# Kernel tuning notes

Measured on AMD Instinct MI355X. Metric: run time of the kernel, lower is better.

The kernel has to match this reference:

```python
import jax, jax.numpy as jnp
import numpy as np

GRID_SIZE = 5
SPLINE_ORDER = 3
GRID_RANGE = (-1.0, 1.0)
BN_EPS = 1e-5


def _make_grid():
    h = (GRID_RANGE[1] - GRID_RANGE[0]) / GRID_SIZE
    # grid_size + 2*spline_order + 1 = 12 knots, shared across the 9 patch features
    return jnp.arange(-SPLINE_ORDER, GRID_SIZE + SPLINE_ORDER + 1, dtype=jnp.float32) * h + GRID_RANGE[0]


def _b_splines(x, grid):
    # x: (N, F) -> (N, F, grid_size + spline_order) via Cox-de Boor recursion
    x = x[..., None]
    bases = ((x >= grid[:-1]) & (x < grid[1:])).astype(x.dtype)
    for k in range(1, SPLINE_ORDER + 1):
        left = (x - grid[: -(k + 1)]) / (grid[k:-1] - grid[: -(k + 1)]) * bases[..., :-1]
        right = (grid[k + 1:] - x) / (grid[k + 1:] - grid[1:-k]) * bases[..., 1:]
        bases = left + right
    return bases


def setup_inputs() -> dict:
    key = jax.random.key(0)
    ks = jax.random.split(key, 4)
    B, C, H, W = 4, 64, 96, 96
    return {
        "x": jax.random.normal(ks[0], (B, C, H, W), dtype=jnp.float32),
        "base_weight": jax.random.normal(ks[1], (1, 9), dtype=jnp.float32) * 0.3,
        "spline_weight": jax.random.normal(ks[2], (1, 9, GRID_SIZE + SPLINE_ORDER), dtype=jnp.float32) * 0.3,
        "spline_scaler": jax.random.normal(ks[3], (1, 9), dtype=jnp.float32) * 0.3 + 1.0,
        "bn_gamma": jnp.ones((C,), dtype=jnp.float32),
        "bn_beta": jnp.zeros((C,), dtype=jnp.float32),
    }


def reference(x, base_weight, spline_weight, spline_scaler, bn_gamma, bn_beta):
    B, C, H, W = x.shape
    grid = _make_grid()
    # Per-channel depthwise 3x3 patch extraction (pad 1, stride 1), shared KANLinear(9 -> 1)
    patches = jax.lax.conv_general_dilated_patches(
        x.reshape(B * C, 1, H, W), (3, 3), (1, 1), [(1, 1), (1, 1)]
    )  # (B*C, 9, H, W)
    tok = patches.transpose(0, 2, 3, 1).reshape(-1, 9)  # (N, 9)

    base_out = jax.nn.silu(tok) @ base_weight.T  # (N, 1)
    bases = _b_splines(tok, grid)  # (N, 9, 8)
    scaled_sw = (spline_weight * spline_scaler[..., None]).reshape(1, -1)  # (1, 72)
    spline_out = bases.reshape(tok.shape[0], -1) @ scaled_sw.T  # (N, 1)

    y = (base_out + spline_out).reshape(B, C, H, W)

    # BatchNorm2d (training-mode batch statistics) + ReLU
    mean = y.mean(axis=(0, 2, 3))
    var = y.var(axis=(0, 2, 3))
    y_hat = (y - mean[None, :, None, None]) * jax.lax.rsqrt(var + BN_EPS)[None, :, None, None]
    out = jax.nn.relu(y_hat * bn_gamma[None, :, None, None] + bn_beta[None, :, None, None])
    return out
```

## Files before the change

### kernel.cpp

```cpp
#include <hip/hip_runtime.h>
#include <math.h>

#define HH 96
#define WW 96
#define CC 64
#define BB 4
#define PLANE (HH * WW)
#define NPLANES (BB * CC)
#define NPC (BB * PLANE)
#define TILE 32
#define TPL 3
#define NTILES (TPL * TPL)
#define HALO 34
#define HALO_N (HALO * HALO)
#define BLOCK 256


__global__ __launch_bounds__(BLOCK) void kconv_stage1(
    const float* __restrict__ x,
    const float* __restrict__ base_w,
    const float* __restrict__ spline_w,
    const float* __restrict__ spline_s,
    float* __restrict__ y,
    float2* __restrict__ part)
{
    __shared__ float4 s_c[9 * 13];
    __shared__ float  s_bw[9];
    __shared__ float2 s_g[HALO_N];

    const int tid = threadIdx.x;

    if (tid < 9 * 13) {
        const int j  = tid / 13;
        const int ip = tid - j * 13;
        const int p  = ip - 1;
        const float sc = spline_s[j];
        float w[4];
#pragma unroll
        for (int r = 0; r < 4; ++r) {
            const int q = p - 3 + r;
            w[r] = (q >= 0 && q < 8) ? spline_w[j * 8 + q] * sc : 0.0f;
        }
        float4 c;
        c.x = (w[0] + 4.0f * w[1] + w[2]) * (1.0f / 6.0f);
        c.y = (w[2] - w[0]) * 0.5f;
        c.z = (w[0] - 2.0f * w[1] + w[2]) * 0.5f;
        c.w = (w[3] - w[0]) * (1.0f / 6.0f) + (w[1] - w[2]) * 0.5f;
        s_c[tid] = c;
    }
    if (tid < 9) s_bw[tid] = base_w[tid];

    const int plane = blockIdx.z;
    const int h0 = blockIdx.y * TILE;
    const int w0 = blockIdx.x * TILE;
    const float* xp = x + (size_t)plane * PLANE;

    for (int i = tid; i < HALO_N; i += BLOCK) {
        const int hy = i / HALO;
        const int hx = i - hy * HALO;
        const int gh = h0 + hy - 1;
        const int gw = w0 + hx - 1;
        float v = 0.0f;
        if (gh >= 0 && gh < HH && gw >= 0 && gw < WW) v = xp[gh * WW + gw];
        const float e = __expf(-v);
        const float silu = v * __builtin_amdgcn_rcpf(1.0f + e);
        float s = (v + 2.2f) * 2.5f;
        s = fminf(fmaxf(s, -0.5f), 11.5f);
        s_g[i] = make_float2(silu, s);
    }
    __syncthreads();

    const int tx  = tid & 31;
    const int ty4 = (tid >> 5) * 4;

    float lsum = 0.0f, lsq = 0.0f;
    float* yp = y + (size_t)plane * PLANE + (size_t)h0 * WW + w0;

#pragma unroll
    for (int k = 0; k < 4; ++k) {
        const int ty = ty4 + k;
        float acc = 0.0f;
#pragma unroll
        for (int dh = 0; dh < 3; ++dh) {
#pragma unroll
            for (int dw = 0; dw < 3; ++dw) {
                const int j = dh * 3 + dw;
                const float2 g = s_g[(ty + dh) * HALO + (tx + dw)];
                acc = fmaf(s_bw[j], g.x, acc);
                const float pf = floorf(g.y);
                const float u  = g.y - pf;
                const int  ipv = (int)pf + 1;
                const float4 c = s_c[j * 13 + ipv];
                float t = fmaf(c.w, u, c.z);
                t = fmaf(t, u, c.y);
                t = fmaf(t, u, c.x);
                acc += t;
            }
        }
        yp[ty * WW + tx] = acc;
        lsum += acc;
        lsq = fmaf(acc, acc, lsq);
    }

#pragma unroll
    for (int off = 32; off; off >>= 1) {
        lsum += __shfl_down(lsum, off, 64);
        lsq  += __shfl_down(lsq,  off, 64);
    }
    __shared__ float2 red[4];
    if ((tid & 63) == 0) red[tid >> 6] = make_float2(lsum, lsq);
    __syncthreads();
    if (tid == 0) {
        const float s = red[0].x + red[1].x + red[2].x + red[3].x;
        const float q = red[0].y + red[1].y + red[2].y + red[3].y;
        part[plane * NTILES + blockIdx.y * TPL + blockIdx.x] = make_float2(s, q);
    }
}

__global__ __launch_bounds__(BLOCK) void kconv_stage2(
    float* __restrict__ y,
    const float2* __restrict__ part,
    const float* __restrict__ gamma,
    const float* __restrict__ beta)
{
    __shared__ float2 sb;
    const int tid = threadIdx.x;
    const int plane = blockIdx.x;
    const int c = plane & (CC - 1);

    if (tid < 64) {
        float s = 0.0f, q = 0.0f;
        if (tid < 36) {
            const int b = tid / 9;
            const int t = tid - b * 9;
            const float2 pp = part[(c + CC * b) * NTILES + t];
            s = pp.x; q = pp.y;
        }
#pragma unroll
        for (int off = 32; off; off >>= 1) {
            s += __shfl_down(s, off, 64);
            q += __shfl_down(q, off, 64);
        }
        if (tid == 0) {
            const float inv = 1.0f / (float)NPC;
            const float mean = s * inv;
            const float var  = q * inv - mean * mean;
            const float sc   = rsqrtf(var + 1e-5f) * gamma[c];
            sb = make_float2(sc, beta[c] - mean * sc);
        }
    }
    __syncthreads();
    const float2 sbv = sb;

    float4* yp = (float4*)(y + (size_t)plane * PLANE + (size_t)blockIdx.y * 1024);
    float4 v = yp[tid];
    v.x = fmaxf(fmaf(v.x, sbv.x, sbv.y), 0.0f);
    v.y = fmaxf(fmaf(v.y, sbv.x, sbv.y), 0.0f);
    v.z = fmaxf(fmaf(v.z, sbv.x, sbv.y), 0.0f);
    v.w = fmaxf(fmaf(v.w, sbv.x, sbv.y), 0.0f);
    yp[tid] = v;
}

extern "C" void kernel_launch(void* const* d_in, const int* in_sizes, int n_in,
                              void* d_out, int out_size, void* d_ws, size_t ws_size,
                              hipStream_t stream)
{
    const float* x        = (const float*)d_in[0];
    const float* base_w   = (const float*)d_in[1];
    const float* spline_w = (const float*)d_in[2];
    const float* spline_s = (const float*)d_in[3];
    const float* gamma    = (const float*)d_in[4];
    const float* beta     = (const float*)d_in[5];
    float* out   = (float*)d_out;
    float2* part = (float2*)d_ws;

    dim3 g1(TPL, TPL, NPLANES);
    kconv_stage1<<<g1, BLOCK, 0, stream>>>(x, base_w, spline_w, spline_s, out, part);

    dim3 g2(NPLANES, PLANE / (BLOCK * 4));
    kconv_stage2<<<g2, BLOCK, 0, stream>>>(out, part, gamma, beta);
}
```

Measured before the change: 90.68 us.

## Precompute per-pixel fp16 B-spline basis vectors and use packed dot2 accumulation

Rather than storing a clamped spline coordinate and looking up per-interval cubic coefficients, each halo pixel now computes its four cubic B-spline basis values once. These are packed as fp16 pairs into an 8-wide vector aligned to the spline weights, and the output is accumulated with fdot2 against fp16-packed weights held in scalar registers. The accumulation loop is also restructured so each halo row loaded from LDS is reused across the four output rows. This removes repeated floor/index/table-lookup work per tap but doubles LDS traffic per pixel (uint4 + float), drops the input clamp, and lowers spline precision to fp16.

```diff
diff --git a/kernel.cpp b/kernel.cpp
--- a/kernel.cpp
+++ b/kernel.cpp
@@ -15,6 +15,23 @@
 #define HALO_N (HALO * HALO)
 #define BLOCK 256
 
+typedef _Float16 h2v __attribute__((ext_vector_type(2)));
+
+static __device__ __forceinline__ float dot2h(unsigned a, unsigned b, float c) {
+#if __has_builtin(__builtin_amdgcn_fdot2)
+    return __builtin_amdgcn_fdot2(__builtin_bit_cast(h2v, a),
+                                  __builtin_bit_cast(h2v, b), c, false);
+#else
+    h2v x = __builtin_bit_cast(h2v, a);
+    h2v y = __builtin_bit_cast(h2v, b);
+    return c + (float)x[0] * (float)y[0] + (float)x[1] * (float)y[1];
+#endif
+}
+
+static __device__ __forceinline__ unsigned pk16(float a, float b) {
+    return __builtin_bit_cast(unsigned, __builtin_amdgcn_cvt_pkrtz(a, b));
+}
+
 
 __global__ __launch_bounds__(BLOCK) void kconv_stage1(
     const float* __restrict__ x,
@@ -24,29 +41,20 @@
     float* __restrict__ y,
     float2* __restrict__ part)
 {
-    __shared__ float4 s_c[9 * 13];
+    __shared__ uint4  s_n[HALO_N];
+    __shared__ float  s_sl[HALO_N];
+    __shared__ unsigned s_wp[36];
     __shared__ float  s_bw[9];
-    __shared__ float2 s_g[HALO_N];
 
     const int tid = threadIdx.x;
 
-    if (tid < 9 * 13) {
-        const int j  = tid / 13;
-        const int ip = tid - j * 13;
-        const int p  = ip - 1;
+    if (tid < 36) {
+        const int j = tid >> 2;
+        const int k = tid & 3;
         const float sc = spline_s[j];
-        float w[4];
-#pragma unroll
-        for (int r = 0; r < 4; ++r) {
-            const int q = p - 3 + r;
-            w[r] = (q >= 0 && q < 8) ? spline_w[j * 8 + q] * sc : 0.0f;
-        }
-        float4 c;
-        c.x = (w[0] + 4.0f * w[1] + w[2]) * (1.0f / 6.0f);
-        c.y = (w[2] - w[0]) * 0.5f;
-        c.z = (w[0] - 2.0f * w[1] + w[2]) * 0.5f;
-        c.w = (w[3] - w[0]) * (1.0f / 6.0f) + (w[1] - w[2]) * 0.5f;
-        s_c[tid] = c;
+        const float w0 = spline_w[j * 8 + 2 * k]     * sc;
+        const float w1 = spline_w[j * 8 + 2 * k + 1] * sc;
+        s_wp[tid] = pk16(w0, w1);
     }
     if (tid < 9) s_bw[tid] = base_w[tid];
 
@@ -62,44 +70,98 @@
         const int gw = w0 + hx - 1;
         float v = 0.0f;
         if (gh >= 0 && gh < HH && gw >= 0 && gw < WW) v = xp[gh * WW + gw];
-        const float e = __expf(-v);
-        const float silu = v * __builtin_amdgcn_rcpf(1.0f + e);
-        float s = (v + 2.2f) * 2.5f;
-        s = fminf(fmaxf(s, -0.5f), 11.5f);
-        s_g[i] = make_float2(silu, s);
+
+        const float e  = __expf(-v);
+        const float sl = v * __builtin_amdgcn_rcpf(1.0f + e);
+
+        const float sp = fmaf(v, 2.5f, 2.5f);
+        const float tf = floorf(sp);
+        const float u  = sp - tf;
+        const int   t  = (int)tf;
+        const int   m  = t >> 1;
+        const bool  odd = (t & 1) != 0;
+
+        const float w1m = 1.0f - u;
+        const float u2 = u * u;
+        const float u3 = u2 * u;
+        const float B0 = w1m * w1m * (w1m * (1.0f / 6.0f));
+        const float B3 = u2 * (u * (1.0f / 6.0f));
+        const float B1 = fmaf(-u2, 1.0f, fmaf(u3, 0.5f, 2.0f / 3.0f));
+        const float B2 = 1.0f - B0 - B1 - B3;
+
+        const unsigned h01 = pk16(B0, B1);
+        const unsigned h23 = pk16(B2, B3);
+
+        unsigned n[4];
+        unsigned a_prev;
+        {
+            const int k0 = -1 - m;
+            a_prev = (k0 == 0) ? h01 : ((k0 == 1) ? h23 : 0u);
+        }
+#pragma unroll
+        for (int d = 0; d < 4; ++d) {
+            const int k0 = d - m;
+            const unsigned a_cur = (k0 == 0) ? h01 : ((k0 == 1) ? h23 : 0u);
+            const unsigned sh = __builtin_amdgcn_alignbit(a_cur, a_prev, 16);
+            n[d] = odd ? sh : a_cur;
+            a_prev = a_cur;
+        }
+
+        s_n[i]  = make_uint4(n[0], n[1], n[2], n[3]);
+        s_sl[i] = sl;
     }
     __syncthreads();
+
+    unsigned wp[36];
+    float bw[9];
+#pragma unroll
+    for (int q = 0; q < 36; ++q)
+        wp[q] = __builtin_amdgcn_readfirstlane(s_wp[q]);
+#pragma unroll
+    for (int q = 0; q < 9; ++q)
+        bw[q] = __int_as_float(__builtin_amdgcn_readfirstlane(__float_as_int(s_bw[q])));
 
     const int tx  = tid & 31;
     const int ty4 = (tid >> 5) * 4;
 
+    float acc[4] = {0.0f, 0.0f, 0.0f, 0.0f};
+
+#pragma unroll
+    for (int r = 0; r < 6; ++r) {
+        const int base = (ty4 + r) * HALO + tx;
+        uint4 cn[3];
+        float cs[3];
+#pragma unroll
+        for (int dw = 0; dw < 3; ++dw) {
+            cn[dw] = s_n[base + dw];
+            cs[dw] = s_sl[base + dw];
+        }
+#pragma unroll
+        for (int k = 0; k < 4; ++k) {
+            const int dh = r - k;
+            if (dh >= 0 && dh < 3) {
+#pragma unroll
+                for (int dw = 0; dw < 3; ++dw) {
+                    const int j = dh * 3 + dw;
+                    float a = acc[k];
+                    a = dot2h(cn[dw].x, wp[j * 4 + 0], a);
+                    a = dot2h(cn[dw].y, wp[j * 4 + 1], a);
+                    a = dot2h(cn[dw].z, wp[j * 4 + 2], a);
+                    a = dot2h(cn[dw].w, wp[j * 4 + 3], a);
+                    a = fmaf(bw[j], cs[dw], a);
+                    acc[k] = a;
+                }
+            }
+        }
+    }
+
     float lsum = 0.0f, lsq = 0.0f;
     float* yp = y + (size_t)plane * PLANE + (size_t)h0 * WW + w0;
-
 #pragma unroll
     for (int k = 0; k < 4; ++k) {
-        const int ty = ty4 + k;
-        float acc = 0.0f;
-#pragma unroll
-        for (int dh = 0; dh < 3; ++dh) {
-#pragma unroll
-            for (int dw = 0; dw < 3; ++dw) {
-                const int j = dh * 3 + dw;
-                const float2 g = s_g[(ty + dh) * HALO + (tx + dw)];
-                acc = fmaf(s_bw[j], g.x, acc);
-                const float pf = floorf(g.y);
-                const float u  = g.y - pf;
-                const int  ipv = (int)pf + 1;
-                const float4 c = s_c[j * 13 + ipv];
-                float t = fmaf(c.w, u, c.z);
-                t = fmaf(t, u, c.y);
-                t = fmaf(t, u, c.x);
-                acc += t;
-            }
-        }
-        yp[ty * WW + tx] = acc;
-        lsum += acc;
-        lsq = fmaf(acc, acc, lsq);
+        yp[(ty4 + k) * WW + tx] = acc[k];
+        lsum += acc[k];
+        lsq = fmaf(acc[k], acc[k], lsq);
     }
 
 #pragma unroll
```

Measured after the change: 86.60 us. 1.05x faster.
